# Performance work log

Hardware: AMD Instinct MI355X
Metric: run time of the kernel (lower is better)

## Reference

```python
import jax, jax.numpy as jnp
import numpy as np
import math

DIM = 512

def setup_inputs() -> dict:
    key = jax.random.key(0)
    k1, k2, k3, k4 = jax.random.split(key, 4)
    B, SD, SE, D = 32, 512, 512, DIM
    padded_seqs = jax.random.normal(k1, (B, SD, D), dtype=jnp.float32)
    encoder_padded_seqs = jax.random.normal(k2, (B, SE, D), dtype=jnp.float32)
    decoder_mask = jnp.ones((B, SD, 1), dtype=jnp.float32)
    # attention linear: Linear(2*D, D) -> weight (D, 2*D), bias (D,)
    bound = 1.0 / math.sqrt(2 * D)
    W = jax.random.uniform(k3, (D, 2 * D), dtype=jnp.float32, minval=-bound, maxval=bound)
    b = jax.random.uniform(k4, (D,), dtype=jnp.float32, minval=-bound, maxval=bound)
    return {"padded_seqs": padded_seqs, "encoder_padded_seqs": encoder_padded_seqs,
            "decoder_mask": decoder_mask, "W": W, "b": b}

def reference(padded_seqs, encoder_padded_seqs, decoder_mask, W, b):
    D = padded_seqs.shape[-1]
    scale = 1.0 / math.sqrt(D)
    # scores: (B, seq_d, seq_e) via matmul instead of broadcast multiply-sum
    scores = jnp.einsum('bqd,bkd->bqk', padded_seqs, encoder_padded_seqs) * scale
    attention_weights = jax.nn.softmax(scores, axis=2)
    attention_context = jnp.einsum('bqk,bkd->bqd', attention_weights, encoder_padded_seqs)
    cat = jnp.concatenate([padded_seqs, attention_context], axis=2)  # (B, seq_d, 2D)
    attention_masked = jnp.tanh(cat @ W.T + b) * decoder_mask
    return (attention_masked, attention_weights)
```

## Files before the change

### kernel.cpp

```cpp
#include <hip/hip_runtime.h>
#include <math.h>

typedef unsigned short u16;
typedef unsigned int   u32;
typedef __attribute__((ext_vector_type(8))) short bf16x8;
typedef __attribute__((ext_vector_type(4))) float f32x4;

#define BATCH  32
#define SEQ    512
#define DM     512
#define SQE    (SEQ*DM)
#define NBE    ((size_t)BATCH*SQE)

__device__ __forceinline__ u16 f2bf(float x) {
  union { float f; u32 i; } v; v.f = x;
  u32 r = v.i + 0x7fffu + ((v.i >> 16) & 1u);
  return (u16)(r >> 16);
}
__device__ __forceinline__ float bf2f(u16 u) {
  union { u32 i; float f; } v; v.i = ((u32)u) << 16; return v.f;
}
__device__ __forceinline__ float fast_tanh(float x) {
  float xc = fminf(fmaxf(x, -15.f), 15.f);
  float e  = __expf(2.f * xc);
  return (e - 1.f) * __builtin_amdgcn_rcpf(e + 1.f);
}

__device__ __forceinline__ void async16(const void* g, void* l) {
  __builtin_amdgcn_global_load_lds(
      (const __attribute__((address_space(1))) void*)g,
      (__attribute__((address_space(3))) void*)l, 16, 0, 0);
}

#define MFMA(a, b, c) __builtin_amdgcn_mfma_f32_16x16x32_bf16((a), (b), (c), 0, 0, 0)

__device__ __forceinline__ void gemm_bf16(
    const u16* Alo, const u16* Ahi, int ktlo, int kttot, int lda,
    const u16* B, int ldb,
    u16* sA, u16* sB, f32x4 acc[4][4])
{
  const int tid  = threadIdx.x;
  const int lane = tid & 63;
  const int wid  = tid >> 6;
  const int wm = (wid >> 1) * 64;
  const int wn = (wid & 1) * 64;
  const int lm = lane & 15;
  const int lq = lane >> 4;

  size_t aoq[4], boq[4];
#pragma unroll
  for (int q = 0; q < 4; ++q) {
    const int c  = tid + 256 * q;
    const int r  = c >> 3;
    const int kg = ((c & 7) ^ (r & 7)) * 8;
    aoq[q] = (size_t)r * lda + kg;
    boq[q] = (size_t)r * ldb + kg;
  }

#define STAGE_TILE(kt, h)                                                  \
  do {                                                                     \
    const u16* Ab = ((kt) < ktlo) ? (Alo + (size_t)(kt) * 64)              \
                                  : (Ahi + (size_t)((kt) - ktlo) * 64);    \
    const u16* Bb = B + (size_t)(kt) * 64;                                 \
    _Pragma("unroll")                                                      \
    for (int q = 0; q < 4; ++q) {                                          \
      u16* dA = sA + (h) * 8192 + (256 * q + wid * 64) * 8;                \
      u16* dB = sB + (h) * 8192 + (256 * q + wid * 64) * 8;                \
      async16(Ab + aoq[q], dA);                                            \
      async16(Bb + boq[q], dB);                                            \
    }                                                                      \
  } while (0)

  STAGE_TILE(0, 0);
  __syncthreads();
  int cur = 0;
  for (int kt = 0; kt < kttot; ++kt) {
    if (kt + 1 < kttot) STAGE_TILE(kt + 1, cur ^ 1);
    const u16* tA = sA + cur * 8192;
    const u16* tB = sB + cur * 8192;
#pragma unroll
    for (int kk = 0; kk < 2; ++kk) {
      bf16x8 af[4], bv[4];
#pragma unroll
      for (int i = 0; i < 4; ++i) {
        const int R = wm + i * 16 + lm;
        af[i] = *(const bf16x8*)(tA + R * 64 + ((kk * 4 + lq) ^ (R & 7)) * 8);
      }
#pragma unroll
      for (int j = 0; j < 4; ++j) {
        const int R = wn + j * 16 + lm;
        bv[j] = *(const bf16x8*)(tB + R * 64 + ((kk * 4 + lq) ^ (R & 7)) * 8);
      }
#pragma unroll
      for (int i = 0; i < 4; ++i)
#pragma unroll
        for (int j = 0; j < 4; ++j)
          acc[i][j] = MFMA(af[i], bv[j], acc[i][j]);
    }
    __syncthreads();
    cur ^= 1;
  }
#undef STAGE_TILE
}

__global__ __launch_bounds__(256) void k_prep(const float* __restrict__ P,
                                              const float* __restrict__ W,
                                              const float* __restrict__ E,
                                              u16* __restrict__ Pbf,
                                              u16* __restrict__ Wbf,
                                              u16* __restrict__ Ebf,
                                              u16* __restrict__ EbfT,
                                              float* __restrict__ Rsum)
{
  __shared__ u16 sT[64][72];
  const int bx  = blockIdx.x;
  const int tid = threadIdx.x;
  if (bx == 6400) {
    float4 z = {0.f, 0.f, 0.f, 0.f};
#pragma unroll
    for (int j = 0; j < 16; ++j)
      *(float4*)(Rsum + tid * 64 + j * 4) = z;
    return;
  }
  if (bx < 4352) {
    size_t base = (size_t)bx * 2048 + tid * 8;
    const float* s; u16* d;
    if (bx < 4096) { s = P + base; d = Pbf + base; }
    else { size_t o = base - (size_t)4096 * 2048; s = W + o; d = Wbf + o; }
    float4 a = *(const float4*)s;
    float4 b = *(const float4*)(s + 4);
    bf16x8 v;
    v[0] = (short)f2bf(a.x); v[1] = (short)f2bf(a.y);
    v[2] = (short)f2bf(a.z); v[3] = (short)f2bf(a.w);
    v[4] = (short)f2bf(b.x); v[5] = (short)f2bf(b.y);
    v[6] = (short)f2bf(b.z); v[7] = (short)f2bf(b.w);
    *(bf16x8*)d = v;
    return;
  }
  const int e  = bx - 4352;
  const int b  = e >> 6;
  const int s0 = ((e >> 3) & 7) * 64;
  const int d0 = (e & 7) * 64;
  const int r = tid >> 2, c = (tid & 3) * 16;
  const float* src = E + (size_t)b * SQE + (size_t)(s0 + r) * DM + d0 + c;
  float4 x0 = ((const float4*)src)[0];
  float4 x1 = ((const float4*)src)[1];
  float4 x2 = ((const float4*)src)[2];
  float4 x3 = ((const float4*)src)[3];
  float xs[16] = {x0.x,x0.y,x0.z,x0.w, x1.x,x1.y,x1.z,x1.w,
                  x2.x,x2.y,x2.z,x2.w, x3.x,x3.y,x3.z,x3.w};
  u16 v[16];
#pragma unroll
  for (int j = 0; j < 16; ++j) v[j] = f2bf(xs[j]);
  bf16x8 o0, o1;
#pragma unroll
  for (int j = 0; j < 8; ++j) { o0[j] = (short)v[j]; o1[j] = (short)v[8 + j]; }
  u16* dro = Ebf + (size_t)b * SQE + (size_t)(s0 + r) * DM + d0 + c;
  *(bf16x8*)dro = o0;
  *(bf16x8*)(dro + 8) = o1;
#pragma unroll
  for (int j = 0; j < 16; ++j) sT[c + j][r] = v[j];
  __syncthreads();
  const int dr = tid >> 2, sc = (tid & 3) * 16;
  bf16x8 t0, t1;
#pragma unroll
  for (int j = 0; j < 8; ++j) { t0[j] = (short)sT[dr][sc + j]; t1[j] = (short)sT[dr][sc + 8 + j]; }
  u16* dst = EbfT + (size_t)b * SQE + (size_t)(d0 + dr) * SEQ + s0 + sc;
  *(bf16x8*)dst = t0;
  *(bf16x8*)(dst + 8) = t1;
}

__global__ __launch_bounds__(256) void k_scores(const u16* __restrict__ Pbf,
                                                const u16* __restrict__ Ebf,
                                                u16* __restrict__ Px,
                                                float* __restrict__ Rsum)
{
  __shared__ u16 sA[2 * 128 * 64];
  __shared__ u16 sB[2 * 128 * 64];
  const int mt = blockIdx.x, nt = blockIdx.y, b = blockIdx.z;
  const u16* A = Pbf + (size_t)b * SQE + (size_t)(mt * 128) * DM;
  const u16* B = Ebf + (size_t)b * SQE + (size_t)(nt * 128) * DM;
  f32x4 acc[4][4] = {};
  gemm_bf16(A, A, 8, 8, DM, B, DM, sA, sB, acc);

  const int tid = threadIdx.x, lane = tid & 63, wid = tid >> 6;
  const int wm = (wid >> 1) * 64, wn = (wid & 1) * 64;
  const int lm = lane & 15, lq = lane >> 4;
  const float scale = 0.044194173824159216f;
  u16* out = Px + (size_t)b * SQE + (size_t)(mt * 128) * SEQ + nt * 128;
#pragma unroll
  for (int i = 0; i < 4; ++i)
#pragma unroll
    for (int r = 0; r < 4; ++r) {
      const int row = wm + i * 16 + lq * 4 + r;
      float rs = 0.f;
#pragma unroll
      for (int j = 0; j < 4; ++j) {
        const float p = __expf(acc[i][j][r] * scale);
        out[(size_t)row * SEQ + wn + j * 16 + lm] = f2bf(p);
        rs += p;
      }
      rs += __shfl_xor(rs, 1, 64);
      rs += __shfl_xor(rs, 2, 64);
      rs += __shfl_xor(rs, 4, 64);
      rs += __shfl_xor(rs, 8, 64);
      if (lm == 0)
        atomicAdd(&Rsum[(size_t)b * SEQ + mt * 128 + row], rs);
    }
}

__global__ __launch_bounds__(256) void v_norm(const u16* __restrict__ Px,
                                              const float* __restrict__ Rsum,
                                              float* __restrict__ Wt,
                                              float* __restrict__ Rsinv)
{
  const int row  = blockIdx.x * 4 + (threadIdx.x >> 6);
  const int lane = threadIdx.x & 63;
  const float inv = 1.0f / Rsum[row];
  if (lane == 0) Rsinv[row] = inv;
  bf16x8 v = *(const bf16x8*)(Px + (size_t)row * SEQ + lane * 8);
  float* dst = Wt + (size_t)row * SEQ + lane * 8;
  float4 o0 = {bf2f((u16)v[0]) * inv, bf2f((u16)v[1]) * inv,
               bf2f((u16)v[2]) * inv, bf2f((u16)v[3]) * inv};
  float4 o1 = {bf2f((u16)v[4]) * inv, bf2f((u16)v[5]) * inv,
               bf2f((u16)v[6]) * inv, bf2f((u16)v[7]) * inv};
  *(float4*)(dst)     = o0;
  *(float4*)(dst + 4) = o1;
}

__global__ __launch_bounds__(256) void k_context(const u16* __restrict__ Px,
                                                 const u16* __restrict__ EbfT,
                                                 const float* __restrict__ Rsinv,
                                                 u16* __restrict__ Ctx)
{
  __shared__ u16 sA[2 * 128 * 64];
  __shared__ u16 sB[2 * 128 * 64];
  const int mt = blockIdx.x, nt = blockIdx.y, b = blockIdx.z;
  const u16* A = Px   + (size_t)b * SQE + (size_t)(mt * 128) * SEQ;
  const u16* B = EbfT + (size_t)b * SQE + (size_t)(nt * 128) * SEQ;
  f32x4 acc[4][4] = {};
  gemm_bf16(A, A, 8, 8, SEQ, B, SEQ, sA, sB, acc);

  const int tid = threadIdx.x, lane = tid & 63, wid = tid >> 6;
  const int wm = (wid >> 1) * 64, wn = (wid & 1) * 64;
  const int lm = lane & 15, lq = lane >> 4;
  u16* out = Ctx + (size_t)b * SQE + (size_t)(mt * 128) * DM + nt * 128;
#pragma unroll
  for (int i = 0; i < 4; ++i)
#pragma unroll
    for (int r = 0; r < 4; ++r) {
      const int row = wm + i * 16 + lq * 4 + r;
      const float inv = Rsinv[(size_t)b * SEQ + mt * 128 + row];
#pragma unroll
      for (int j = 0; j < 4; ++j)
        out[(size_t)row * DM + wn + j * 16 + lm] = f2bf(acc[i][j][r] * inv);
    }
}

__global__ __launch_bounds__(256) void k_final(const u16* __restrict__ Pbf,
                                               const u16* __restrict__ Ctx,
                                               const u16* __restrict__ Wbf,
                                               const float* __restrict__ bias,
                                               const float* __restrict__ mask,
                                               float* __restrict__ Out)
{
  __shared__ u16 sA[2 * 128 * 64];
  __shared__ u16 sB[2 * 128 * 64];
  const int mt = blockIdx.x, nt = blockIdx.y, b = blockIdx.z;
  const u16* Alo = Pbf + (size_t)b * SQE + (size_t)(mt * 128) * DM;
  const u16* Ahi = Ctx + (size_t)b * SQE + (size_t)(mt * 128) * DM;
  const u16* B   = Wbf + (size_t)(nt * 128) * 1024;
  f32x4 acc[4][4] = {};
  gemm_bf16(Alo, Ahi, 8, 16, DM, B, 1024, sA, sB, acc);

  const int tid = threadIdx.x, lane = tid & 63, wid = tid >> 6;
  const int wm = (wid >> 1) * 64, wn = (wid & 1) * 64;
  const int lm = lane & 15, lq = lane >> 4;
  float* out = Out + (size_t)b * SQE + (size_t)(mt * 128) * DM + nt * 128;
#pragma unroll
  for (int i = 0; i < 4; ++i)
#pragma unroll
    for (int r = 0; r < 4; ++r) {
      const int row = wm + i * 16 + lq * 4 + r;
      const float mv = mask[b * SEQ + mt * 128 + row];
#pragma unroll
      for (int j = 0; j < 4; ++j) {
        const int col = wn + j * 16 + lm;
        out[(size_t)row * DM + col] = fast_tanh(acc[i][j][r] + bias[nt * 128 + col]) * mv;
      }
    }
}

extern "C" void kernel_launch(void* const* d_in, const int* in_sizes, int n_in,
                              void* d_out, int out_size, void* d_ws, size_t ws_size,
                              hipStream_t stream)
{
  int i8a = -1, i8b = -1, iM = -1, iW = -1, iB = -1;
  for (int i = 0; i < n_in; ++i) {
    const int s = in_sizes[i];
    if (s == BATCH * SQE)      { if (i8a < 0) i8a = i; else i8b = i; }
    else if (s == BATCH * SEQ) iM = i;
    else if (s == DM * 1024)   iW = i;
    else if (s == DM)          iB = i;
  }
  if (i8a < 0) i8a = 0;
  if (i8b < 0) i8b = 1;
  if (iM < 0) iM = 2;
  if (iW < 0) iW = 3;
  if (iB < 0) iB = 4;
  const float* P  = (const float*)d_in[i8a];
  const float* E  = (const float*)d_in[i8b];
  const float* Mk = (const float*)d_in[iM];
  const float* W  = (const float*)d_in[iW];
  const float* Bi = (const float*)d_in[iB];

  float* out0 = (float*)d_out;
  float* out1 = out0 + NBE;

  u16*   Pbf   = (u16*)d_ws;
  u16*   Ebf   = Pbf  + NBE;
  u16*   EbfT  = Ebf  + NBE;
  u16*   Ctx   = EbfT + NBE;
  u16*   Wbf   = Ctx  + NBE;
  float* Rsum  = (float*)(Wbf + 524288);
  float* Rsinv = Rsum + 16384;
  u16*   Px    = (u16*)(Rsinv + 16384);

  dim3 blk(256);
  dim3 gg(4, 4, BATCH);
  k_prep   <<<dim3(6401), blk, 0, stream>>>(P, W, E, Pbf, Wbf, Ebf, EbfT, Rsum);
  k_scores <<<gg, blk, 0, stream>>>(Pbf, Ebf, Px, Rsum);
  v_norm   <<<dim3(BATCH * SEQ / 4), blk, 0, stream>>>(Px, Rsum, out1, Rsinv);
  k_context<<<gg, blk, 0, stream>>>(Px, EbfT, Rsinv, Ctx);
  k_final  <<<gg, blk, 0, stream>>>(Pbf, Ctx, Wbf, Bi, Mk, out0);
}
```

Before: 200.0 us.

## Fuse pipeline into one cooperative kernel with grid syncs and partial row sums

Folds the prep, scores, context and final GEMM stages into a single cooperative kernel of 512 blocks that separates the phases with grid-wide syncs. The atomic row-sum accumulation and its zeroing are replaced by per-tile partial sums, which the context phase reduces. The separate normalization kernel that wrote the attention weights is merged into the context phase. This removes launch gaps and atomics, but it limits the prep phase to 512 resident blocks looping over work and adds grid-barrier cost. If the cooperative launch fails, the code falls back to four ordinary launches.

```diff
diff --git a/kernel.cpp b/kernel.cpp
--- a/kernel.cpp
+++ b/kernel.cpp
@@ -1,5 +1,8 @@
 #include <hip/hip_runtime.h>
+#include <hip/hip_cooperative_groups.h>
 #include <math.h>
+
+namespace cg = cooperative_groups;
 
 typedef unsigned short u16;
 typedef unsigned int   u32;
@@ -103,40 +106,28 @@
 #undef STAGE_TILE
 }
 
-__global__ __launch_bounds__(256) void k_prep(const float* __restrict__ P,
-                                              const float* __restrict__ W,
-                                              const float* __restrict__ E,
-                                              u16* __restrict__ Pbf,
-                                              u16* __restrict__ Wbf,
-                                              u16* __restrict__ Ebf,
-                                              u16* __restrict__ EbfT,
-                                              float* __restrict__ Rsum)
-{
-  __shared__ u16 sT[64][72];
-  const int bx  = blockIdx.x;
+__device__ __forceinline__ void phase_prep(
+    int bx, const float* P, const float* W, const float* E,
+    u16* Pbf, u16* Wbf, u16* Ebf, u16* EbfT, u16* smem)
+{
   const int tid = threadIdx.x;
-  if (bx == 6400) {
-    float4 z = {0.f, 0.f, 0.f, 0.f};
-#pragma unroll
-    for (int j = 0; j < 16; ++j)
-      *(float4*)(Rsum + tid * 64 + j * 4) = z;
-    return;
-  }
   if (bx < 4352) {
     size_t base = (size_t)bx * 2048 + tid * 8;
     const float* s; u16* d;
     if (bx < 4096) { s = P + base; d = Pbf + base; }
     else { size_t o = base - (size_t)4096 * 2048; s = W + o; d = Wbf + o; }
     float4 a = *(const float4*)s;
-    float4 b = *(const float4*)(s + 4);
+    float4 b4 = *(const float4*)(s + 4);
     bf16x8 v;
     v[0] = (short)f2bf(a.x); v[1] = (short)f2bf(a.y);
     v[2] = (short)f2bf(a.z); v[3] = (short)f2bf(a.w);
-    v[4] = (short)f2bf(b.x); v[5] = (short)f2bf(b.y);
-    v[6] = (short)f2bf(b.z); v[7] = (short)f2bf(b.w);
+    v[4] = (short)f2bf(b4.x); v[5] = (short)f2bf(b4.y);
+    v[6] = (short)f2bf(b4.z); v[7] = (short)f2bf(b4.w);
     *(bf16x8*)d = v;
     return;
   }
+  u16 (*sT)[72] = (u16(*)[72])smem;
+  __syncthreads();
   const int e  = bx - 4352;
   const int b  = e >> 6;
   const int s0 = ((e >> 3) & 7) * 64;
@@ -170,24 +161,22 @@
   *(bf16x8*)(dst + 8) = t1;
 }
 
-__global__ __launch_bounds__(256) void k_scores(const u16* __restrict__ Pbf,
-                                                const u16* __restrict__ Ebf,
-                                                u16* __restrict__ Px,
-                                                float* __restrict__ Rsum)
-{
-  __shared__ u16 sA[2 * 128 * 64];
-  __shared__ u16 sB[2 * 128 * 64];
-  const int mt = blockIdx.x, nt = blockIdx.y, b = blockIdx.z;
-  const u16* A = Pbf + (size_t)b * SQE + (size_t)(mt * 128) * DM;
-  const u16* B = Ebf + (size_t)b * SQE + (size_t)(nt * 128) * DM;
+__device__ __forceinline__ void phase_scores(
+    int bid, const u16* Pbf, const u16* Ebf, u16* Px, float* Rpart, u16* smem)
+{
+  u16* sA = smem; u16* sB = smem + 16384;
+  const int mt = bid & 3, nt = (bid >> 2) & 3, b = bid >> 4;
+  const u16* A  = Pbf + (size_t)b * SQE + (size_t)(mt * 128) * DM;
+  const u16* Bp = Ebf + (size_t)b * SQE + (size_t)(nt * 128) * DM;
   f32x4 acc[4][4] = {};
-  gemm_bf16(A, A, 8, 8, DM, B, DM, sA, sB, acc);
+  gemm_bf16(A, A, 8, 8, DM, Bp, DM, sA, sB, acc);
 
   const int tid = threadIdx.x, lane = tid & 63, wid = tid >> 6;
   const int wm = (wid >> 1) * 64, wn = (wid & 1) * 64;
   const int lm = lane & 15, lq = lane >> 4;
   const float scale = 0.044194173824159216f;
-  u16* out = Px + (size_t)b * SQE + (size_t)(mt * 128) * SEQ + nt * 128;
+  u16* outp = Px + (size_t)b * SQE + (size_t)(mt * 128) * SEQ + nt * 128;
+  float* rp = Rpart + (size_t)(nt * 2 + (wid & 1)) * 16384 + (size_t)b * SEQ + mt * 128;
 #pragma unroll
   for (int i = 0; i < 4; ++i)
 #pragma unroll
@@ -197,81 +186,78 @@
 #pragma unroll
       for (int j = 0; j < 4; ++j) {
         const float p = __expf(acc[i][j][r] * scale);
-        out[(size_t)row * SEQ + wn + j * 16 + lm] = f2bf(p);
+        outp[(size_t)row * SEQ + wn + j * 16 + lm] = f2bf(p);
         rs += p;
       }
       rs += __shfl_xor(rs, 1, 64);
       rs += __shfl_xor(rs, 2, 64);
       rs += __shfl_xor(rs, 4, 64);
       rs += __shfl_xor(rs, 8, 64);
-      if (lm == 0)
-        atomicAdd(&Rsum[(size_t)b * SEQ + mt * 128 + row], rs);
+      if (lm == 0) rp[row] = rs;
     }
 }
 
-__global__ __launch_bounds__(256) void v_norm(const u16* __restrict__ Px,
-                                              const float* __restrict__ Rsum,
-                                              float* __restrict__ Wt,
-                                              float* __restrict__ Rsinv)
-{
-  const int row  = blockIdx.x * 4 + (threadIdx.x >> 6);
-  const int lane = threadIdx.x & 63;
-  const float inv = 1.0f / Rsum[row];
-  if (lane == 0) Rsinv[row] = inv;
-  bf16x8 v = *(const bf16x8*)(Px + (size_t)row * SEQ + lane * 8);
-  float* dst = Wt + (size_t)row * SEQ + lane * 8;
-  float4 o0 = {bf2f((u16)v[0]) * inv, bf2f((u16)v[1]) * inv,
-               bf2f((u16)v[2]) * inv, bf2f((u16)v[3]) * inv};
-  float4 o1 = {bf2f((u16)v[4]) * inv, bf2f((u16)v[5]) * inv,
-               bf2f((u16)v[6]) * inv, bf2f((u16)v[7]) * inv};
-  *(float4*)(dst)     = o0;
-  *(float4*)(dst + 4) = o1;
-}
-
-__global__ __launch_bounds__(256) void k_context(const u16* __restrict__ Px,
-                                                 const u16* __restrict__ EbfT,
-                                                 const float* __restrict__ Rsinv,
-                                                 u16* __restrict__ Ctx)
-{
-  __shared__ u16 sA[2 * 128 * 64];
-  __shared__ u16 sB[2 * 128 * 64];
-  const int mt = blockIdx.x, nt = blockIdx.y, b = blockIdx.z;
-  const u16* A = Px   + (size_t)b * SQE + (size_t)(mt * 128) * SEQ;
-  const u16* B = EbfT + (size_t)b * SQE + (size_t)(nt * 128) * SEQ;
+__device__ __forceinline__ void phase_ctx(
+    int bid, const u16* Px, const u16* EbfT, const float* Rpart,
+    u16* Ctx, float* out1, u16* smem)
+{
+  u16* sA = smem; u16* sB = smem + 16384;
+  const int mt = bid & 3, nt = (bid >> 2) & 3, b = bid >> 4;
+  const u16* A  = Px   + (size_t)b * SQE + (size_t)(mt * 128) * SEQ;
+  const u16* Bp = EbfT + (size_t)b * SQE + (size_t)(nt * 128) * SEQ;
   f32x4 acc[4][4] = {};
-  gemm_bf16(A, A, 8, 8, SEQ, B, SEQ, sA, sB, acc);
+  gemm_bf16(A, A, 8, 8, SEQ, Bp, SEQ, sA, sB, acc);
 
   const int tid = threadIdx.x, lane = tid & 63, wid = tid >> 6;
   const int wm = (wid >> 1) * 64, wn = (wid & 1) * 64;
   const int lm = lane & 15, lq = lane >> 4;
-  u16* out = Ctx + (size_t)b * SQE + (size_t)(mt * 128) * DM + nt * 128;
+  float* sInv = (float*)smem;
+  if (tid < 128) {
+    const size_t row = (size_t)b * SEQ + mt * 128 + tid;
+    float s = 0.f;
+#pragma unroll
+    for (int p = 0; p < 8; ++p) s += Rpart[(size_t)p * 16384 + row];
+    sInv[tid] = 1.0f / s;
+  }
+  __syncthreads();
+  u16* outc = Ctx + (size_t)b * SQE + (size_t)(mt * 128) * DM + nt * 128;
 #pragma unroll
   for (int i = 0; i < 4; ++i)
 #pragma unroll
     for (int r = 0; r < 4; ++r) {
-      const int row = wm + i * 16 + lq * 4 + r;
-      const float inv = Rsinv[(size_t)b * SEQ + mt * 128 + row];
+      const int rl = wm + i * 16 + lq * 4 + r;
+      const float inv = sInv[rl];
 #pragma unroll
       for (int j = 0; j < 4; ++j)
-        out[(size_t)row * DM + wn + j * 16 + lm] = f2bf(acc[i][j][r] * inv);
+        outc[(size_t)rl * DM + wn + j * 16 + lm] = f2bf(acc[i][j][r] * inv);
     }
-}
-
-__global__ __launch_bounds__(256) void k_final(const u16* __restrict__ Pbf,
-                                               const u16* __restrict__ Ctx,
-                                               const u16* __restrict__ Wbf,
-                                               const float* __restrict__ bias,
-                                               const float* __restrict__ mask,
-                                               float* __restrict__ Out)
-{
-  __shared__ u16 sA[2 * 128 * 64];
-  __shared__ u16 sB[2 * 128 * 64];
-  const int mt = blockIdx.x, nt = blockIdx.y, b = blockIdx.z;
+  const int rr = tid >> 1, cb = (tid & 1) * 64;
+  const float inv2 = sInv[rr];
+  const u16* src = Px + (size_t)b * SQE + (size_t)(mt * 128 + rr) * SEQ + nt * 128 + cb;
+  float* dst = out1 + (size_t)b * SQE + (size_t)(mt * 128 + rr) * SEQ + nt * 128 + cb;
+#pragma unroll
+  for (int j = 0; j < 8; ++j) {
+    bf16x8 v = *(const bf16x8*)(src + j * 8);
+    float4 o0 = {bf2f((u16)v[0]) * inv2, bf2f((u16)v[1]) * inv2,
+                 bf2f((u16)v[2]) * inv2, bf2f((u16)v[3]) * inv2};
+    float4 o1 = {bf2f((u16)v[4]) * inv2, bf2f((u16)v[5]) * inv2,
+                 bf2f((u16)v[6]) * inv2, bf2f((u16)v[7]) * inv2};
+    *(float4*)(dst + j * 8)     = o0;
+    *(float4*)(dst + j * 8 + 4) = o1;
+  }
+}
+
+__device__ __forceinline__ void phase_final(
+    int bid, const u16* Pbf, const u16* Ctx, const u16* Wbf,
+    const float* Bi, const float* Mk, float* Out, u16* smem)
+{
+  u16* sA = smem; u16* sB = smem + 16384;
+  const int mt = bid & 3, nt = (bid >> 2) & 3, b = bid >> 4;
   const u16* Alo = Pbf + (size_t)b * SQE + (size_t)(mt * 128) * DM;
   const u16* Ahi = Ctx + (size_t)b * SQE + (size_t)(mt * 128) * DM;
-  const u16* B   = Wbf + (size_t)(nt * 128) * 1024;
+  const u16* Bp  = Wbf + (size_t)(nt * 128) * 1024;
   f32x4 acc[4][4] = {};
-  gemm_bf16(Alo, Ahi, 8, 16, DM, B, 1024, sA, sB, acc);
+  gemm_bf16(Alo, Ahi, 8, 16, DM, Bp, 1024, sA, sB, acc);
 
   const int tid = threadIdx.x, lane = tid & 63, wid = tid >> 6;
   const int wm = (wid >> 1) * 64, wn = (wid & 1) * 64;
@@ -282,13 +268,58 @@
 #pragma unroll
     for (int r = 0; r < 4; ++r) {
       const int row = wm + i * 16 + lq * 4 + r;
-      const float mv = mask[b * SEQ + mt * 128 + row];
+      const float mv = Mk[b * SEQ + mt * 128 + row];
 #pragma unroll
       for (int j = 0; j < 4; ++j) {
         const int col = wn + j * 16 + lm;
-        out[(size_t)row * DM + col] = fast_tanh(acc[i][j][r] + bias[nt * 128 + col]) * mv;
+        out[(size_t)row * DM + col] = fast_tanh(acc[i][j][r] + Bi[nt * 128 + col]) * mv;
       }
     }
+}
+
+__global__ __launch_bounds__(256) void k_mega(
+    const float* __restrict__ P, const float* __restrict__ W,
+    const float* __restrict__ E, const float* __restrict__ Mk,
+    const float* __restrict__ Bi,
+    u16* Pbf, u16* Wbf, u16* Ebf, u16* EbfT,
+    float* Rpart, u16* Px, u16* Ctx,
+    float* out0, float* out1)
+{
+  __shared__ u16 smem[32768];
+  cg::grid_group g = cg::this_grid();
+  for (int bx = blockIdx.x; bx < 6400; bx += 512)
+    phase_prep(bx, P, W, E, Pbf, Wbf, Ebf, EbfT, smem);
+  g.sync();
+  phase_scores(blockIdx.x, Pbf, Ebf, Px, Rpart, smem);
+  g.sync();
+  phase_ctx(blockIdx.x, Px, EbfT, Rpart, Ctx, out1, smem);
+  g.sync();
+  phase_final(blockIdx.x, Pbf, Ctx, Wbf, Bi, Mk, out0, smem);
+}
+
+__global__ __launch_bounds__(256) void k_p1(const float* P, const float* W, const float* E,
+                                            u16* Pbf, u16* Wbf, u16* Ebf, u16* EbfT)
+{
+  __shared__ u16 sT[64 * 72];
+  phase_prep(blockIdx.x, P, W, E, Pbf, Wbf, Ebf, EbfT, sT);
+}
+__global__ __launch_bounds__(256) void k_p2(const u16* Pbf, const u16* Ebf,
+                                            u16* Px, float* Rpart)
+{
+  __shared__ u16 smem[32768];
+  phase_scores(blockIdx.x, Pbf, Ebf, Px, Rpart, smem);
+}
+__global__ __launch_bounds__(256) void k_p3(const u16* Px, const u16* EbfT,
+                                            const float* Rpart, u16* Ctx, float* out1)
+{
+  __shared__ u16 smem[32768];
+  phase_ctx(blockIdx.x, Px, EbfT, Rpart, Ctx, out1, smem);
+}
+__global__ __launch_bounds__(256) void k_p4(const u16* Pbf, const u16* Ctx, const u16* Wbf,
+                                            const float* Bi, const float* Mk, float* out0)
+{
+  __shared__ u16 smem[32768];
+  phase_final(blockIdx.x, Pbf, Ctx, Wbf, Bi, Mk, out0, smem);
 }
 
 extern "C" void kernel_launch(void* const* d_in, const int* in_sizes, int n_in,
@@ -321,16 +352,21 @@
   u16*   Ebf   = Pbf  + NBE;
   u16*   EbfT  = Ebf  + NBE;
   u16*   Ctx   = EbfT + NBE;
-  u16*   Wbf   = Ctx  + NBE;
-  float* Rsum  = (float*)(Wbf + 524288);
-  float* Rsinv = Rsum + 16384;
-  u16*   Px    = (u16*)(Rsinv + 16384);
-
-  dim3 blk(256);
-  dim3 gg(4, 4, BATCH);
-  k_prep   <<<dim3(6401), blk, 0, stream>>>(P, W, E, Pbf, Wbf, Ebf, EbfT, Rsum);
-  k_scores <<<gg, blk, 0, stream>>>(Pbf, Ebf, Px, Rsum);
-  v_norm   <<<dim3(BATCH * SEQ / 4), blk, 0, stream>>>(Px, Rsum, out1, Rsinv);
-  k_context<<<gg, blk, 0, stream>>>(Px, EbfT, Rsinv, Ctx);
-  k_final  <<<gg, blk, 0, stream>>>(Pbf, Ctx, Wbf, Bi, Mk, out0);
-}
+  u16*   Px    = Ctx  + NBE;
+  u16*   Wbf   = Px   + NBE;
+  float* Rpart = (float*)(Wbf + 524288);
+
+  void* ka[] = {(void*)&P, (void*)&W, (void*)&E, (void*)&Mk, (void*)&Bi,
+                (void*)&Pbf, (void*)&Wbf, (void*)&Ebf, (void*)&EbfT,
+                (void*)&Rpart, (void*)&Px, (void*)&Ctx,
+                (void*)&out0, (void*)&out1};
+  hipError_t err = hipLaunchCooperativeKernel((const void*)k_mega, dim3(512),
+                                              dim3(256), ka, 0, stream);
+  if (err != hipSuccess) {
+    (void)hipGetLastError();
+    k_p1<<<dim3(6400), dim3(256), 0, stream>>>(P, W, E, Pbf, Wbf, Ebf, EbfT);
+    k_p2<<<dim3(512),  dim3(256), 0, stream>>>(Pbf, Ebf, Px, Rpart);
+    k_p3<<<dim3(512),  dim3(256), 0, stream>>>(Px, EbfT, Rpart, Ctx, out1);
+    k_p4<<<dim3(512),  dim3(256), 0, stream>>>(Pbf, Ctx, Wbf, Bi, Mk, out0);
+  }
+}
```

Result: slower. 430.9 us (+115.5%).

## Fuse softmax normalization into context kernel and replace atomics with partial sums

Applied to the files above, without the earlier changes.

Row sums from the scores kernel are now written as per-(column-tile, wave) partials instead of atomically accumulated, which removes the zeroing block in the prep kernel. The context kernel reduces the partials into shared memory and also writes the normalized fp32 attention weights for its tile. This removes the separate v_norm launch and its extra read of Px. In exchange, the context kernel epilogue gets longer and takes an extra barrier.

```diff
diff --git a/kernel.cpp b/kernel.cpp
--- a/kernel.cpp
+++ b/kernel.cpp
@@ -109,19 +109,11 @@
                                               u16* __restrict__ Pbf,
                                               u16* __restrict__ Wbf,
                                               u16* __restrict__ Ebf,
-                                              u16* __restrict__ EbfT,
-                                              float* __restrict__ Rsum)
+                                              u16* __restrict__ EbfT)
 {
   __shared__ u16 sT[64][72];
   const int bx  = blockIdx.x;
   const int tid = threadIdx.x;
-  if (bx == 6400) {
-    float4 z = {0.f, 0.f, 0.f, 0.f};
-#pragma unroll
-    for (int j = 0; j < 16; ++j)
-      *(float4*)(Rsum + tid * 64 + j * 4) = z;
-    return;
-  }
   if (bx < 4352) {
     size_t base = (size_t)bx * 2048 + tid * 8;
     const float* s; u16* d;
@@ -173,21 +165,22 @@
 __global__ __launch_bounds__(256) void k_scores(const u16* __restrict__ Pbf,
                                                 const u16* __restrict__ Ebf,
                                                 u16* __restrict__ Px,
-                                                float* __restrict__ Rsum)
+                                                float* __restrict__ Rpart)
 {
   __shared__ u16 sA[2 * 128 * 64];
   __shared__ u16 sB[2 * 128 * 64];
   const int mt = blockIdx.x, nt = blockIdx.y, b = blockIdx.z;
-  const u16* A = Pbf + (size_t)b * SQE + (size_t)(mt * 128) * DM;
-  const u16* B = Ebf + (size_t)b * SQE + (size_t)(nt * 128) * DM;
+  const u16* A  = Pbf + (size_t)b * SQE + (size_t)(mt * 128) * DM;
+  const u16* Bp = Ebf + (size_t)b * SQE + (size_t)(nt * 128) * DM;
   f32x4 acc[4][4] = {};
-  gemm_bf16(A, A, 8, 8, DM, B, DM, sA, sB, acc);
+  gemm_bf16(A, A, 8, 8, DM, Bp, DM, sA, sB, acc);
 
   const int tid = threadIdx.x, lane = tid & 63, wid = tid >> 6;
   const int wm = (wid >> 1) * 64, wn = (wid & 1) * 64;
   const int lm = lane & 15, lq = lane >> 4;
   const float scale = 0.044194173824159216f;
-  u16* out = Px + (size_t)b * SQE + (size_t)(mt * 128) * SEQ + nt * 128;
+  u16* outp = Px + (size_t)b * SQE + (size_t)(mt * 128) * SEQ + nt * 128;
+  float* rp = Rpart + (size_t)(nt * 2 + (wid & 1)) * 16384 + (size_t)b * SEQ + mt * 128;
 #pragma unroll
   for (int i = 0; i < 4; ++i)
 #pragma unroll
@@ -197,64 +190,68 @@
 #pragma unroll
       for (int j = 0; j < 4; ++j) {
         const float p = __expf(acc[i][j][r] * scale);
-        out[(size_t)row * SEQ + wn + j * 16 + lm] = f2bf(p);
+        outp[(size_t)row * SEQ + wn + j * 16 + lm] = f2bf(p);
         rs += p;
       }
       rs += __shfl_xor(rs, 1, 64);
       rs += __shfl_xor(rs, 2, 64);
       rs += __shfl_xor(rs, 4, 64);
       rs += __shfl_xor(rs, 8, 64);
-      if (lm == 0)
-        atomicAdd(&Rsum[(size_t)b * SEQ + mt * 128 + row], rs);
+      if (lm == 0) rp[row] = rs;
     }
-}
-
-__global__ __launch_bounds__(256) void v_norm(const u16* __restrict__ Px,
-                                              const float* __restrict__ Rsum,
-                                              float* __restrict__ Wt,
-                                              float* __restrict__ Rsinv)
-{
-  const int row  = blockIdx.x * 4 + (threadIdx.x >> 6);
-  const int lane = threadIdx.x & 63;
-  const float inv = 1.0f / Rsum[row];
-  if (lane == 0) Rsinv[row] = inv;
-  bf16x8 v = *(const bf16x8*)(Px + (size_t)row * SEQ + lane * 8);
-  float* dst = Wt + (size_t)row * SEQ + lane * 8;
-  float4 o0 = {bf2f((u16)v[0]) * inv, bf2f((u16)v[1]) * inv,
-               bf2f((u16)v[2]) * inv, bf2f((u16)v[3]) * inv};
-  float4 o1 = {bf2f((u16)v[4]) * inv, bf2f((u16)v[5]) * inv,
-               bf2f((u16)v[6]) * inv, bf2f((u16)v[7]) * inv};
-  *(float4*)(dst)     = o0;
-  *(float4*)(dst + 4) = o1;
 }
 
 __global__ __launch_bounds__(256) void k_context(const u16* __restrict__ Px,
                                                  const u16* __restrict__ EbfT,
-                                                 const float* __restrict__ Rsinv,
-                                                 u16* __restrict__ Ctx)
+                                                 const float* __restrict__ Rpart,
+                                                 u16* __restrict__ Ctx,
+                                                 float* __restrict__ out1)
 {
   __shared__ u16 sA[2 * 128 * 64];
   __shared__ u16 sB[2 * 128 * 64];
   const int mt = blockIdx.x, nt = blockIdx.y, b = blockIdx.z;
-  const u16* A = Px   + (size_t)b * SQE + (size_t)(mt * 128) * SEQ;
-  const u16* B = EbfT + (size_t)b * SQE + (size_t)(nt * 128) * SEQ;
+  const u16* A  = Px   + (size_t)b * SQE + (size_t)(mt * 128) * SEQ;
+  const u16* Bp = EbfT + (size_t)b * SQE + (size_t)(nt * 128) * SEQ;
   f32x4 acc[4][4] = {};
-  gemm_bf16(A, A, 8, 8, SEQ, B, SEQ, sA, sB, acc);
+  gemm_bf16(A, A, 8, 8, SEQ, Bp, SEQ, sA, sB, acc);
 
   const int tid = threadIdx.x, lane = tid & 63, wid = tid >> 6;
   const int wm = (wid >> 1) * 64, wn = (wid & 1) * 64;
   const int lm = lane & 15, lq = lane >> 4;
-  u16* out = Ctx + (size_t)b * SQE + (size_t)(mt * 128) * DM + nt * 128;
+  float* sInv = (float*)sA;
+  if (tid < 128) {
+    const size_t row = (size_t)b * SEQ + mt * 128 + tid;
+    float s = 0.f;
+#pragma unroll
+    for (int p = 0; p < 8; ++p) s += Rpart[(size_t)p * 16384 + row];
+    sInv[tid] = 1.0f / s;
+  }
+  __syncthreads();
+  u16* outc = Ctx + (size_t)b * SQE + (size_t)(mt * 128) * DM + nt * 128;
 #pragma unroll
   for (int i = 0; i < 4; ++i)
 #pragma unroll
     for (int r = 0; r < 4; ++r) {
-      const int row = wm + i * 16 + lq * 4 + r;
-      const float inv = Rsinv[(size_t)b * SEQ + mt * 128 + row];
+      const int rl = wm + i * 16 + lq * 4 + r;
+      const float inv = sInv[rl];
 #pragma unroll
       for (int j = 0; j < 4; ++j)
-        out[(size_t)row * DM + wn + j * 16 + lm] = f2bf(acc[i][j][r] * inv);
+        outc[(size_t)rl * DM + wn + j * 16 + lm] = f2bf(acc[i][j][r] * inv);
     }
+  const int rr = tid >> 1, cb = (tid & 1) * 64;
+  const float inv2 = sInv[rr];
+  const u16* src = Px + (size_t)b * SQE + (size_t)(mt * 128 + rr) * SEQ + nt * 128 + cb;
+  float* dst = out1 + (size_t)b * SQE + (size_t)(mt * 128 + rr) * SEQ + nt * 128 + cb;
+#pragma unroll
+  for (int j = 0; j < 8; ++j) {
+    bf16x8 v = *(const bf16x8*)(src + j * 8);
+    float4 o0 = {bf2f((u16)v[0]) * inv2, bf2f((u16)v[1]) * inv2,
+                 bf2f((u16)v[2]) * inv2, bf2f((u16)v[3]) * inv2};
+    float4 o1 = {bf2f((u16)v[4]) * inv2, bf2f((u16)v[5]) * inv2,
+                 bf2f((u16)v[6]) * inv2, bf2f((u16)v[7]) * inv2};
+    *(float4*)(dst + j * 8)     = o0;
+    *(float4*)(dst + j * 8 + 4) = o1;
+  }
 }
 
 __global__ __launch_bounds__(256) void k_final(const u16* __restrict__ Pbf,
@@ -269,9 +266,9 @@
   const int mt = blockIdx.x, nt = blockIdx.y, b = blockIdx.z;
   const u16* Alo = Pbf + (size_t)b * SQE + (size_t)(mt * 128) * DM;
   const u16* Ahi = Ctx + (size_t)b * SQE + (size_t)(mt * 128) * DM;
-  const u16* B   = Wbf + (size_t)(nt * 128) * 1024;
+  const u16* Bp  = Wbf + (size_t)(nt * 128) * 1024;
   f32x4 acc[4][4] = {};
-  gemm_bf16(Alo, Ahi, 8, 16, DM, B, 1024, sA, sB, acc);
+  gemm_bf16(Alo, Ahi, 8, 16, DM, Bp, 1024, sA, sB, acc);
 
   const int tid = threadIdx.x, lane = tid & 63, wid = tid >> 6;
   const int wm = (wid >> 1) * 64, wn = (wid & 1) * 64;
@@ -321,16 +318,14 @@
   u16*   Ebf   = Pbf  + NBE;
   u16*   EbfT  = Ebf  + NBE;
   u16*   Ctx   = EbfT + NBE;
-  u16*   Wbf   = Ctx  + NBE;
-  float* Rsum  = (float*)(Wbf + 524288);
-  float* Rsinv = Rsum + 16384;
-  u16*   Px    = (u16*)(Rsinv + 16384);
+  u16*   Px    = Ctx  + NBE;
+  u16*   Wbf   = Px   + NBE;
+  float* Rpart = (float*)(Wbf + 524288);
 
   dim3 blk(256);
   dim3 gg(4, 4, BATCH);
-  k_prep   <<<dim3(6401), blk, 0, stream>>>(P, W, E, Pbf, Wbf, Ebf, EbfT, Rsum);
-  k_scores <<<gg, blk, 0, stream>>>(Pbf, Ebf, Px, Rsum);
-  v_norm   <<<dim3(BATCH * SEQ / 4), blk, 0, stream>>>(Px, Rsum, out1, Rsinv);
-  k_context<<<gg, blk, 0, stream>>>(Px, EbfT, Rsinv, Ctx);
+  k_prep   <<<dim3(6400), blk, 0, stream>>>(P, W, E, Pbf, Wbf, Ebf, EbfT);
+  k_scores <<<gg, blk, 0, stream>>>(Pbf, Ebf, Px, Rpart);
+  k_context<<<gg, blk, 0, stream>>>(Px, EbfT, Rpart, Ctx, out1);
   k_final  <<<gg, blk, 0, stream>>>(Pbf, Ctx, Wbf, Bi, Mk, out0);
 }
```

Result: no change. 202.1 us (+1.1%).
